# Kernel optimization log

Measured on AMD Instinct MI355X. Metric: run time of the kernel, lower is better.

Reference implementation:

```python
import jax, jax.numpy as jnp
import numpy as np

B, S, H = 4, 2048, 3072
NQ, NKV, D = 16, 8, 256
NEG = -2.3819763e38  # large negative for masking


def setup_inputs() -> dict:
    key = jax.random.key(0)
    ks = jax.random.split(key, 8)
    hidden_states = jax.random.normal(ks[0], (B, S, H), dtype=jnp.float32)
    # rotary frequencies: angle theta per (pos, dim-pair), Gemma-style base 10000
    inv_freq = 1.0 / (10000.0 ** (np.arange(0, D, 2, dtype=np.float32) / D))  # [D/2]
    t = np.arange(S, dtype=np.float32)
    ang = np.outer(t, inv_freq)  # [S, D/2]
    freqs_cos = jnp.broadcast_to(jnp.asarray(np.cos(ang)), (B, S, D // 2)).astype(jnp.float32)
    freqs_sin = jnp.broadcast_to(jnp.asarray(np.sin(ang)), (B, S, D // 2)).astype(jnp.float32)
    # additive causal mask [B,1,S,S]
    causal = jnp.tril(jnp.ones((S, S), dtype=bool))
    mask = jnp.where(causal, 0.0, NEG).astype(jnp.float32)[None, None]
    mask = jnp.broadcast_to(mask, (B, 1, S, S))
    sc = 0.02
    wq = jax.random.normal(ks[1], (NQ * D, H), dtype=jnp.float32) * sc
    wk = jax.random.normal(ks[2], (NKV * D, H), dtype=jnp.float32) * sc
    wv = jax.random.normal(ks[3], (NKV * D, H), dtype=jnp.float32) * sc
    wo = jax.random.normal(ks[4], (H, NQ * D), dtype=jnp.float32) * sc
    return {"hidden_states": hidden_states, "freqs_cos": freqs_cos,
            "freqs_sin": freqs_sin, "mask": mask,
            "wq": wq, "wk": wk, "wv": wv, "wo": wo}


def _apply_rotary(x, cos, sin):
    # x: [B,S,N,Dh]; cos/sin: [B,S,Dh/2]. Complex rotation: (x1 + i x2) * (cos + i sin)
    d2 = x.shape[-1] // 2
    x1, x2 = x[..., :d2], x[..., d2:]
    c = cos[:, :, None, :]
    s = sin[:, :, None, :]
    return jnp.concatenate([x1 * c - x2 * s, x1 * s + x2 * c], axis=-1)


def reference(hidden_states, freqs_cos, freqs_sin, mask, wq, wk, wv, wo):
    b, s, _ = hidden_states.shape
    scaling = D ** -0.5
    xq = (hidden_states @ wq.T).reshape(b, s, NQ, D)
    xk = (hidden_states @ wk.T).reshape(b, s, NKV, D)
    xv = (hidden_states @ wv.T).reshape(b, s, NKV, D)
    xq = _apply_rotary(xq, freqs_cos, freqs_sin)
    xk = _apply_rotary(xk, freqs_cos, freqs_sin)
    # GQA: repeat kv heads to match query heads
    g = NQ // NKV
    xk = jnp.repeat(xk, g, axis=2)  # [b,s,NQ,D]
    xv = jnp.repeat(xv, g, axis=2)
    scores = jnp.einsum('bqhd,bkhd->bhqk', xq * scaling, xk) + mask
    probs = jax.nn.softmax(scores, axis=-1)
    out = jnp.einsum('bhqk,bkhd->bqhd', probs, xv).reshape(b, s, NQ * D)
    return out @ wo.T
```

## Files before the change

### kernel.cpp

```cpp
#include <hip/hip_runtime.h>

#define DEVI __device__ __forceinline__

typedef __attribute__((ext_vector_type(8))) short s16x8;
typedef __attribute__((ext_vector_type(4))) float f32x4;
typedef unsigned short u16;

DEVI u16 f2bf(float f){
  unsigned u = __float_as_uint(f);
  u += 0x7FFFu + ((u >> 16) & 1u);
  return (u16)(u >> 16);
}
DEVI float bf2f(u16 s){ return __uint_as_float(((unsigned)s) << 16); }

DEVI void gload16(const void* g, void* l){
  __builtin_amdgcn_global_load_lds((const __attribute__((address_space(1))) void*)g,
                                   (__attribute__((address_space(3))) void*)l, 16, 0, 0);
}

__global__ __launch_bounds__(256) void cast_bf16_kernel(const float* __restrict__ src,
                                                        u16* __restrict__ dst, int n4){
  int i = blockIdx.x*256 + threadIdx.x;
  if (i < n4){
    float4 v = reinterpret_cast<const float4*>(src)[i];
    ushort4 o;
    o.x = f2bf(v.x); o.y = f2bf(v.y); o.z = f2bf(v.z); o.w = f2bf(v.w);
    reinterpret_cast<ushort4*>(dst)[i] = o;
  }
}

__global__ __launch_bounds__(256) void rope_kernel(u16* __restrict__ X,
                                                   const float* __restrict__ fc,
                                                   const float* __restrict__ fs, int NH){
  int tid = blockIdx.x*256 + threadIdx.x;
  int rr = tid >> 4;
  int d0 = (tid & 15) * 8;
  int s  = rr & 2047;
  int b  = (rr >> 11) / NH;
  size_t base = (size_t)rr * 256;
  s16x8 x1 = *(const s16x8*)&X[base + d0];
  s16x8 x2 = *(const s16x8*)&X[base + 128 + d0];
  const float* cp = fc + ((size_t)(b*2048 + s))*128 + d0;
  const float* sp = fs + ((size_t)(b*2048 + s))*128 + d0;
  alignas(16) u16 o1[8], o2[8];
  #pragma unroll
  for (int j=0;j<8;j++){
    float c = cp[j], sn = sp[j];
    float a = bf2f((u16)x1[j]);
    float bb = bf2f((u16)x2[j]);
    o1[j] = f2bf(a*c - bb*sn);
    o2[j] = f2bf(a*sn + bb*c);
  }
  *(s16x8*)&X[base + d0]       = *(const s16x8*)o1;
  *(s16x8*)&X[base + 128 + d0] = *(const s16x8*)o2;
}

template<int MODE>
__global__ __launch_bounds__(512,2) void gemm8p_kernel(
    const u16* __restrict__ A, const u16* __restrict__ Bw,
    int K, int nbn, int Nn,
    float* __restrict__ Cf, u16* __restrict__ Qo, u16* __restrict__ Ko, u16* __restrict__ Vo)
{
  __shared__ u16 LDSb[2][32768];
  const int nwg = gridDim.x;
  const int bid0 = blockIdx.x;
  const int bid = (bid0 & 7)*(nwg >> 3) + (bid0 >> 3);
  const int bm = bid / nbn, bn = bid % nbn;
  const int t = threadIdx.x, ln = t&63;
  const int wvid = t>>6;
  const int wr = wvid>>2, wc = wvid&3;
  const int frow = ln&15, g = ln>>4;
  const int NT = K >> 6;

  size_t soff[2];
  #pragma unroll
  for (int i=0;i<2;i++){
    const int phys = (i*512 + t)*16;
    const int L = phys ^ (((phys>>7)&7)<<4);
    soff[i] = (size_t)(L >> 7) * K + ((L & 127) >> 1);
  }
  const u16* Apan = A  + (size_t)(bm*256)*K;
  const u16* Bpan = Bw + (size_t)(bn*256)*K;

  int aoff[8][2], boff[4][2];
  #pragma unroll
  for (int mi=0;mi<8;mi++){
    const int row = mi*16 + frow;
    #pragma unroll
    for (int ks=0;ks<2;ks++){
      const int L = row*128 + ks*64 + g*16;
      aoff[mi][ks] = wr*16384 + (L ^ ((row&7)<<4));
    }
  }
  #pragma unroll
  for (int ni=0;ni<4;ni++){
    const int row = (wc&1)*64 + ni*16 + frow;
    #pragma unroll
    for (int ks=0;ks<2;ks++){
      const int L = row*128 + ks*64 + g*16;
      boff[ni][ks] = 32768 + (wc>>1)*16384 + (L ^ ((row&7)<<4));
    }
  }

  f32x4 acc[8][4];
  #pragma unroll
  for (int i=0;i<8;i++)
    #pragma unroll
    for (int j=0;j<4;j++) acc[i][j] = f32x4{0.f,0.f,0.f,0.f};

  auto stageHalf = [&](int buf, int ht, int tstep){
    char* dst = (char*)&LDSb[buf][0] + ht*16384;
    const u16* src = (ht < 2 ? Apan : Bpan) + (size_t)((ht&1)*128)*K + (size_t)tstep*64;
    #pragma unroll
    for (int i=0;i<2;i++)
      gload16(src + soff[i], dst + (i*512 + t)*16);
  };

  stageHalf(0,0,0); stageHalf(0,1,0); stageHalf(0,2,0); stageHalf(0,3,0);
  if (NT > 1){ stageHalf(1,2,1); stageHalf(1,3,1); }
  asm volatile("s_waitcnt vmcnt(4)" ::: "memory");
  __builtin_amdgcn_s_barrier();

  for (int T=0; T<NT; ++T){
    const char* sb = (const char*)&LDSb[T&1][0];
    s16x8 bh[4][2];
    #pragma unroll
    for (int p=0;p<4;++p){
      if (p==0){
        #pragma unroll
        for (int ni=0;ni<4;ni++)
          #pragma unroll
          for (int ks=0;ks<2;ks++)
            bh[ni][ks] = *(const s16x8*)(sb + boff[ni][ks]);
      }
      s16x8 afr[2][2];
      #pragma unroll
      for (int m2=0;m2<2;m2++)
        #pragma unroll
        for (int ks=0;ks<2;ks++)
          afr[m2][ks] = *(const s16x8*)(sb + aoff[p*2+m2][ks]);
      if      (p==0){ if (T+1 < NT) stageHalf((T+1)&1, 0, T+1); }
      else if (p==1){ if (T+1 < NT) stageHalf((T+1)&1, 1, T+1); }
      else if (p==2){ if (T+2 < NT) stageHalf(T&1,     2, T+2); }
      else          { if (T+2 < NT) stageHalf(T&1,     3, T+2); }
      __builtin_amdgcn_s_barrier();
      asm volatile("s_waitcnt lgkmcnt(0)" ::: "memory");
      __builtin_amdgcn_sched_barrier(0);
      __builtin_amdgcn_s_setprio(1);
      #pragma unroll
      for (int ks=0;ks<2;ks++)
        #pragma unroll
        for (int m2=0;m2<2;m2++)
          #pragma unroll
          for (int ni=0;ni<4;ni++)
            acc[p*2+m2][ni] = __builtin_amdgcn_mfma_f32_16x16x32_bf16(
                afr[m2][ks], bh[ni][ks], acc[p*2+m2][ni], 0,0,0);
      __builtin_amdgcn_s_setprio(0);
      __builtin_amdgcn_sched_barrier(0);
      if (p==3){
        if (T+2 < NT)       { asm volatile("s_waitcnt vmcnt(4)" ::: "memory"); }
        else if (T+2 == NT) { asm volatile("s_waitcnt vmcnt(0)" ::: "memory"); }
      }
      __builtin_amdgcn_s_barrier();
    }
  }

  const int mbase = bm*256 + wr*128;
  const int nbase = bn*256 + wc*64;
  #pragma unroll
  for (int mi=0;mi<8;mi++){
    #pragma unroll
    for (int ni=0;ni<4;ni++){
      #pragma unroll
      for (int r=0;r<4;r++){
        const int m = mbase + mi*16 + g*4 + r;
        const int n = nbase + ni*16 + frow;
        if (MODE == 0){
          const int b = m >> 11, s = m & 2047;
          const u16 v = f2bf(acc[mi][ni][r]);
          if (n < 4096){
            const int h = n >> 8, d = n & 255;
            Qo[((((size_t)b*16 + h)*2048 + s) << 8) + d] = v;
          } else if (n < 6144){
            const int n2 = n - 4096; const int h = n2 >> 8, d = n2 & 255;
            Ko[((((size_t)b*8 + h)*2048 + s) << 8) + d] = v;
          } else {
            const int n2 = n - 6144; const int h = n2 >> 8, d = n2 & 255;
            Vo[((((size_t)b*8 + h)*2048 + s) << 8) + d] = v;
          }
        } else {
          Cf[(size_t)m*Nn + n] = acc[mi][ni][r];
        }
      }
    }
  }
}

__global__ __launch_bounds__(512,2) void flash_attn_kernel(
    const u16* __restrict__ Qg, const u16* __restrict__ Kg,
    const u16* __restrict__ Vg, u16* __restrict__ Og)
{
  __shared__ u16 Kl[2][32*256];
  __shared__ u16 Vt[256*40];
  __shared__ u16 Pl[8][16*40];
  const int xb = blockIdx.x;
  const int kvh = blockIdx.y, b = blockIdx.z;
  const int t = threadIdx.x, wvid = t>>6, ln = t&63;
  const int frow = ln&15, g = ln>>4;
  const int qh = kvh*2 + (wvid>>2);
  const u16* Qp = Qg + ((size_t)(b*16 + qh) << 19);
  const u16* Kp = Kg + ((size_t)(b*8 + kvh) << 19);
  const u16* Vp = Vg + ((size_t)(b*8 + kvh) << 19);
  const int vd = t & 255;
  const int vh = (t >> 8) << 4;

  s16x8 ones;
  #pragma unroll
  for (int j=0;j<8;j++) ones[j] = (short)0x3F80;

  #pragma unroll 1
  for (int seg=0; seg<2; seg++){
    const int qb = seg ? (31 - xb) : xb;
    const int q0 = qb*64 + (wvid&3)*16;
    const int ntiles = qb*2 + 2;

    s16x8 aq[8];
    #pragma unroll
    for (int kk=0;kk<8;kk++){
      s16x8 v = *(const s16x8*)&Qp[(size_t)(q0+frow)*256 + kk*32 + g*8];
      #pragma unroll
      for (int j=0;j<8;j++) v[j] = (short)f2bf(bf2f((u16)v[j]) * 0.0625f);
      aq[kk] = v;
    }

    f32x4 accO[16];
    #pragma unroll
    for (int i=0;i<16;i++) accO[i] = f32x4{0.f,0.f,0.f,0.f};
    f32x4 accL = f32x4{0.f,0.f,0.f,0.f};
    float mrow[4] = {-1e30f,-1e30f,-1e30f,-1e30f};

    alignas(16) u16 va[16];

    #pragma unroll
    for (int i=0;i<2;i++){
      const int ci = i*512 + t;
      const int gelem = (ci*8) ^ ((((unsigned)ci>>5)&7)<<3);
      gload16(Kp + gelem, &Kl[0][(ci & ~63)*8]);
    }
    #pragma unroll
    for (int j=0;j<16;j++) va[j] = Vp[(size_t)(vh + j)*256 + vd];
    __syncthreads();
    *(s16x8*)&Vt[vd*40 + vh]     = *(const s16x8*)&va[0];
    *(s16x8*)&Vt[vd*40 + vh + 8] = *(const s16x8*)&va[8];
    __syncthreads();

    for (int kt=0; kt<ntiles; kt++){
      const int kbase = kt*32;
      const bool haveNext = (kt+1 < ntiles);
      if (haveNext){
        const int kb2 = kbase + 32;
        #pragma unroll
        for (int i=0;i<2;i++){
          const int ci = i*512 + t;
          const int gelem = (ci*8) ^ ((((unsigned)ci>>5)&7)<<3);
          gload16(Kp + (size_t)kb2*256 + gelem, &Kl[(kt+1)&1][(ci & ~63)*8]);
        }
        #pragma unroll
        for (int j=0;j<16;j++) va[j] = Vp[(size_t)(kb2 + vh + j)*256 + vd];
      }

      if (kbase <= q0 + 15){
        const char* Kb8 = (const char*)&Kl[kt&1][0];
        f32x4 sc[2];
        sc[0] = f32x4{0.f,0.f,0.f,0.f};
        sc[1] = f32x4{0.f,0.f,0.f,0.f};
        #pragma unroll
        for (int kb=0;kb<2;kb++){
          const int rr = kb*16 + frow;
          const int sw = (rr&7)<<4;
          const int bb = rr*512 + g*16;
          #pragma unroll
          for (int kk=0;kk<8;kk++){
            const s16x8 bk = *(const s16x8*)(Kb8 + ((bb + kk*64) ^ sw));
            sc[kb] = __builtin_amdgcn_mfma_f32_16x16x32_bf16(aq[kk], bk, sc[kb], 0,0,0);
          }
        }
        if (kbase + 31 > q0){
          #pragma unroll
          for (int r=0;r<4;r++){
            const int qrow = q0 + g*4 + r;
            if (kbase + frow > qrow)      sc[0][r] = -1e30f;
            if (kbase + 16 + frow > qrow) sc[1][r] = -1e30f;
          }
        }
        float mx[4];
        #pragma unroll
        for (int r=0;r<4;r++) mx[r] = fmaxf(sc[0][r], sc[1][r]);
        #pragma unroll
        for (int m=1;m<16;m<<=1)
          #pragma unroll
          for (int r=0;r<4;r++)
            mx[r] = fmaxf(mx[r], __shfl_xor(mx[r], m));
        float need = -1.f;
        #pragma unroll
        for (int r=0;r<4;r++) need = fmaxf(need, mx[r] - mrow[r]);
        if (__any(need > 8.0f)){
          #pragma unroll
          for (int r=0;r<4;r++){
            const float mn = fmaxf(mrow[r], mx[r]);
            const float s = __expf(mrow[r] - mn);
            mrow[r] = mn;
            accL[r] *= s;
            #pragma unroll
            for (int nb=0;nb<16;nb++) accO[nb][r] *= s;
          }
        }
        #pragma unroll
        for (int r=0;r<4;r++){
          const float p0 = __expf(sc[0][r] - mrow[r]);
          const float p1 = __expf(sc[1][r] - mrow[r]);
          Pl[wvid][(g*4+r)*40 + frow]      = f2bf(p0);
          Pl[wvid][(g*4+r)*40 + 16 + frow] = f2bf(p1);
        }
        asm volatile("s_waitcnt lgkmcnt(0)" ::: "memory");
        __builtin_amdgcn_sched_barrier(0);
        const s16x8 pf = *(const s16x8*)&Pl[wvid][frow*40 + g*8];
        accL = __builtin_amdgcn_mfma_f32_16x16x32_bf16(pf, ones, accL, 0,0,0);
        #pragma unroll
        for (int nb=0;nb<16;nb++){
          const s16x8 vf = *(const s16x8*)&Vt[(nb*16+frow)*40 + g*8];
          accO[nb] = __builtin_amdgcn_mfma_f32_16x16x32_bf16(pf, vf, accO[nb], 0,0,0);
        }
      }

      __syncthreads();
      if (haveNext){
        *(s16x8*)&Vt[vd*40 + vh]     = *(const s16x8*)&va[0];
        *(s16x8*)&Vt[vd*40 + vh + 8] = *(const s16x8*)&va[8];
      }
      __syncthreads();
    }

    f32x4 rl;
    #pragma unroll
    for (int r=0;r<4;r++) rl[r] = 1.0f / accL[r];
    #pragma unroll
    for (int nb=0;nb<16;nb++)
      #pragma unroll
      for (int r=0;r<4;r++){
        const int qrow = q0 + g*4 + r;
        Og[(((size_t)(b*2048 + qrow)*16 + qh) << 8) + nb*16 + frow] = f2bf(accO[nb][r] * rl[r]);
      }
  }
}

extern "C" void kernel_launch(void* const* d_in, const int* in_sizes, int n_in,
                              void* d_out, int out_size, void* d_ws, size_t ws_size,
                              hipStream_t stream) {
  const float* hidden = (const float*)d_in[0];
  const float* fcos   = (const float*)d_in[1];
  const float* fsin   = (const float*)d_in[2];
  const float* wq = (const float*)d_in[4];
  const float* wk = (const float*)d_in[5];
  const float* wv = (const float*)d_in[6];
  const float* wo = (const float*)d_in[7];
  float* out = (float*)d_out;

  char* ws = (char*)d_ws;
  u16* Xb   = (u16*)(ws);
  u16* Wcat = (u16*)(ws + 50331648);
  u16* Wob  = (u16*)(ws + 100663296);
  u16* Qb   = (u16*)(ws + 125829120);
  u16* Kb   = (u16*)(ws + 192937984);
  u16* Vb   = (u16*)(ws + 226492416);
  u16* AOb  = (u16*)(ws + 260046848);

  cast_bf16_kernel<<<24576, 256, 0, stream>>>(hidden, Xb, 6291456);
  cast_bf16_kernel<<<12288, 256, 0, stream>>>(wq, Wcat,              3145728);
  cast_bf16_kernel<<< 6144, 256, 0, stream>>>(wk, Wcat + 12582912,   1572864);
  cast_bf16_kernel<<< 6144, 256, 0, stream>>>(wv, Wcat + 18874368,   1572864);
  cast_bf16_kernel<<<12288, 256, 0, stream>>>(wo, Wob,               3145728);

  gemm8p_kernel<0><<<32*32, 512, 0, stream>>>(Xb, Wcat, 3072, 32, 8192,
                                              nullptr, Qb, Kb, Vb);

  rope_kernel<<<8192, 256, 0, stream>>>(Qb, fcos, fsin, 16);
  rope_kernel<<<4096, 256, 0, stream>>>(Kb, fcos, fsin, 8);

  flash_attn_kernel<<<dim3(16,8,4), 512, 0, stream>>>(Qb, Kb, Vb, AOb);

  gemm8p_kernel<1><<<32*12, 512, 0, stream>>>(AOb, Wob, 4096, 12, 3072,
                                              out, nullptr, nullptr, nullptr);
}
```

Before: 1.037 ms.

## Store V transposed from QKV GEMM and async-load it in flash attention

The QKV projection GEMM now writes V in a [b,kvh,d,s] transposed layout, staging the tile through LDS with an XOR swizzle so global stores are coalesced. The attention kernel then loads V tiles straight into double-buffered, swizzled LDS with async global_load_lds, as it already does for K. This removes the per-thread scalar strided V loads, the register transpose and one block-wide barrier per KV tile. In exchange the GEMM epilogue for V blocks gains an LDS round trip and barrier, and LDS use in attention rises with the second V buffer.

Measured after the change: 994.4 us. 1.04x faster.

```diff
diff --git a/kernel.cpp b/kernel.cpp
--- a/kernel.cpp
+++ b/kernel.cpp
@@ -167,29 +167,55 @@
 
   const int mbase = bm*256 + wr*128;
   const int nbase = bn*256 + wc*64;
-  #pragma unroll
-  for (int mi=0;mi<8;mi++){
-    #pragma unroll
-    for (int ni=0;ni<4;ni++){
-      #pragma unroll
-      for (int r=0;r<4;r++){
-        const int m = mbase + mi*16 + g*4 + r;
-        const int n = nbase + ni*16 + frow;
-        if (MODE == 0){
-          const int b = m >> 11, s = m & 2047;
-          const u16 v = f2bf(acc[mi][ni][r]);
-          if (n < 4096){
-            const int h = n >> 8, d = n & 255;
-            Qo[((((size_t)b*16 + h)*2048 + s) << 8) + d] = v;
-          } else if (n < 6144){
-            const int n2 = n - 4096; const int h = n2 >> 8, d = n2 & 255;
-            Ko[((((size_t)b*8 + h)*2048 + s) << 8) + d] = v;
+  if (MODE == 0 && bn >= 24){
+    u16* TB = (u16*)&LDSb[0][0];
+    const int h  = bn - 24;
+    const int b  = (bm*256) >> 11;
+    const int s0 = (bm*256) & 2047;
+    #pragma unroll
+    for (int mi=0;mi<8;mi++){
+      #pragma unroll
+      for (int ni=0;ni<4;ni++){
+        const int d  = wc*64 + ni*16 + frow;
+        const int sl = wr*128 + mi*16 + g*4;
+        alignas(8) u16 p4[4];
+        #pragma unroll
+        for (int r=0;r<4;r++) p4[r] = f2bf(acc[mi][ni][r]);
+        const int Tphys = (d*512 + sl*2) ^ ((d&7)<<4);
+        *(uint2*)((char*)TB + Tphys) = *(const uint2*)p4;
+      }
+    }
+    __syncthreads();
+    #pragma unroll
+    for (int i=0;i<16;i++){
+      const int ci = i*512 + t;
+      const int d = ci >> 5, sb2 = (ci & 31)*16;
+      const int phys = (d*512 + sb2) ^ ((d&7)<<4);
+      const s16x8 val = *(const s16x8*)((const char*)TB + phys);
+      *(s16x8*)&Vo[(((size_t)(b*8 + h)*256 + d)*2048) + s0 + (sb2>>1)] = val;
+    }
+  } else {
+    #pragma unroll
+    for (int mi=0;mi<8;mi++){
+      #pragma unroll
+      for (int ni=0;ni<4;ni++){
+        #pragma unroll
+        for (int r=0;r<4;r++){
+          const int m = mbase + mi*16 + g*4 + r;
+          const int n = nbase + ni*16 + frow;
+          if (MODE == 0){
+            const int b = m >> 11, s = m & 2047;
+            const u16 v = f2bf(acc[mi][ni][r]);
+            if (n < 4096){
+              const int h = n >> 8, d = n & 255;
+              Qo[((((size_t)b*16 + h)*2048 + s) << 8) + d] = v;
+            } else {
+              const int n2 = n - 4096; const int h = n2 >> 8, d = n2 & 255;
+              Ko[((((size_t)b*8 + h)*2048 + s) << 8) + d] = v;
+            }
           } else {
-            const int n2 = n - 6144; const int h = n2 >> 8, d = n2 & 255;
-            Vo[((((size_t)b*8 + h)*2048 + s) << 8) + d] = v;
+            Cf[(size_t)m*Nn + n] = acc[mi][ni][r];
           }
-        } else {
-          Cf[(size_t)m*Nn + n] = acc[mi][ni][r];
         }
       }
     }
@@ -198,25 +224,46 @@
 
 __global__ __launch_bounds__(512,2) void flash_attn_kernel(
     const u16* __restrict__ Qg, const u16* __restrict__ Kg,
-    const u16* __restrict__ Vg, u16* __restrict__ Og)
+    const u16* __restrict__ VTg, u16* __restrict__ Og)
 {
   __shared__ u16 Kl[2][32*256];
-  __shared__ u16 Vt[256*40];
+  __shared__ u16 Vt[2][256*32];
   __shared__ u16 Pl[8][16*40];
   const int xb = blockIdx.x;
   const int kvh = blockIdx.y, b = blockIdx.z;
   const int t = threadIdx.x, wvid = t>>6, ln = t&63;
   const int frow = ln&15, g = ln>>4;
   const int qh = kvh*2 + (wvid>>2);
-  const u16* Qp = Qg + ((size_t)(b*16 + qh) << 19);
-  const u16* Kp = Kg + ((size_t)(b*8 + kvh) << 19);
-  const u16* Vp = Vg + ((size_t)(b*8 + kvh) << 19);
-  const int vd = t & 255;
-  const int vh = (t >> 8) << 4;
+  const u16* Qp = Qg  + ((size_t)(b*16 + qh) << 19);
+  const u16* Kp = Kg  + ((size_t)(b*8 + kvh) << 19);
+  const u16* Vp = VTg + ((size_t)(b*8 + kvh) << 19);
 
   s16x8 ones;
   #pragma unroll
   for (int j=0;j<8;j++) ones[j] = (short)0x3F80;
+
+  int kge[2]; int vrow[2]; int vcb[2];
+  #pragma unroll
+  for (int i=0;i<2;i++){
+    const int ci = i*512 + t;
+    kge[i] = (ci*8) ^ ((((unsigned)ci>>5)&7)<<3);
+    const int phys = ci*16;
+    const int L = phys ^ (((phys>>6)&3)<<4);
+    vrow[i] = L >> 6;  vcb[i] = (L & 63) >> 1;
+  }
+
+  auto stageKV = [&](int kbase, int buf){
+    #pragma unroll
+    for (int i=0;i<2;i++){
+      const int ci = i*512 + t;
+      gload16(Kp + (size_t)kbase*256 + kge[i], &Kl[buf][(ci & ~63)*8]);
+    }
+    #pragma unroll
+    for (int i=0;i<2;i++){
+      const int ci = i*512 + t;
+      gload16(Vp + (size_t)vrow[i]*2048 + kbase + vcb[i], &Vt[buf][(ci & ~63)*8]);
+    }
+  };
 
   #pragma unroll 1
   for (int seg=0; seg<2; seg++){
@@ -239,35 +286,12 @@
     f32x4 accL = f32x4{0.f,0.f,0.f,0.f};
     float mrow[4] = {-1e30f,-1e30f,-1e30f,-1e30f};
 
-    alignas(16) u16 va[16];
-
-    #pragma unroll
-    for (int i=0;i<2;i++){
-      const int ci = i*512 + t;
-      const int gelem = (ci*8) ^ ((((unsigned)ci>>5)&7)<<3);
-      gload16(Kp + gelem, &Kl[0][(ci & ~63)*8]);
-    }
-    #pragma unroll
-    for (int j=0;j<16;j++) va[j] = Vp[(size_t)(vh + j)*256 + vd];
-    __syncthreads();
-    *(s16x8*)&Vt[vd*40 + vh]     = *(const s16x8*)&va[0];
-    *(s16x8*)&Vt[vd*40 + vh + 8] = *(const s16x8*)&va[8];
+    stageKV(0, 0);
     __syncthreads();
 
     for (int kt=0; kt<ntiles; kt++){
       const int kbase = kt*32;
-      const bool haveNext = (kt+1 < ntiles);
-      if (haveNext){
-        const int kb2 = kbase + 32;
-        #pragma unroll
-        for (int i=0;i<2;i++){
-          const int ci = i*512 + t;
-          const int gelem = (ci*8) ^ ((((unsigned)ci>>5)&7)<<3);
-          gload16(Kp + (size_t)kb2*256 + gelem, &Kl[(kt+1)&1][(ci & ~63)*8]);
-        }
-        #pragma unroll
-        for (int j=0;j<16;j++) va[j] = Vp[(size_t)(kb2 + vh + j)*256 + vd];
-      }
+      if (kt+1 < ntiles) stageKV(kbase + 32, (kt+1)&1);
 
       if (kbase <= q0 + 15){
         const char* Kb8 = (const char*)&Kl[kt&1][0];
@@ -326,18 +350,15 @@
         __builtin_amdgcn_sched_barrier(0);
         const s16x8 pf = *(const s16x8*)&Pl[wvid][frow*40 + g*8];
         accL = __builtin_amdgcn_mfma_f32_16x16x32_bf16(pf, ones, accL, 0,0,0);
+        const char* Vb8 = (const char*)&Vt[kt&1][0];
         #pragma unroll
         for (int nb=0;nb<16;nb++){
-          const s16x8 vf = *(const s16x8*)&Vt[(nb*16+frow)*40 + g*8];
+          const int row = nb*16 + frow;
+          const s16x8 vf = *(const s16x8*)(Vb8 + ((row*64 + g*16) ^ ((row&3)<<4)));
           accO[nb] = __builtin_amdgcn_mfma_f32_16x16x32_bf16(pf, vf, accO[nb], 0,0,0);
         }
       }
 
-      __syncthreads();
-      if (haveNext){
-        *(s16x8*)&Vt[vd*40 + vh]     = *(const s16x8*)&va[0];
-        *(s16x8*)&Vt[vd*40 + vh + 8] = *(const s16x8*)&va[8];
-      }
       __syncthreads();
     }
 
@@ -372,7 +393,7 @@
   u16* Wob  = (u16*)(ws + 100663296);
   u16* Qb   = (u16*)(ws + 125829120);
   u16* Kb   = (u16*)(ws + 192937984);
-  u16* Vb   = (u16*)(ws + 226492416);
+  u16* VTb  = (u16*)(ws + 226492416);
   u16* AOb  = (u16*)(ws + 260046848);
 
   cast_bf16_kernel<<<24576, 256, 0, stream>>>(hidden, Xb, 6291456);
@@ -382,12 +403,12 @@
   cast_bf16_kernel<<<12288, 256, 0, stream>>>(wo, Wob,               3145728);
 
   gemm8p_kernel<0><<<32*32, 512, 0, stream>>>(Xb, Wcat, 3072, 32, 8192,
-                                              nullptr, Qb, Kb, Vb);
+                                              nullptr, Qb, Kb, VTb);
 
   rope_kernel<<<8192, 256, 0, stream>>>(Qb, fcos, fsin, 16);
   rope_kernel<<<4096, 256, 0, stream>>>(Kb, fcos, fsin, 8);
 
-  flash_attn_kernel<<<dim3(16,8,4), 512, 0, stream>>>(Qb, Kb, Vb, AOb);
+  flash_attn_kernel<<<dim3(16,8,4), 512, 0, stream>>>(Qb, Kb, VTb, AOb);
 
   gemm8p_kernel<1><<<32*12, 512, 0, stream>>>(AOb, Wob, 4096, 12, 3072,
                                               out, nullptr, nullptr, nullptr);
```
